# Optimization experiments

Hardware: AMD Instinct MI355X
Metric: run time of the kernel (lower is better)

The kernel has to match this reference:

```python
import jax, jax.numpy as jnp
import numpy as np

GRADIENT_SCALE = 1.0  # undefined global in the source; standard surrogate scale
ALPHA = 0.9
BETA = 0.8
THRESHOLD = 1.0
FEATURES = 512
UNITS = 1024
TIME = 256
BATCH = 128

@jax.custom_vjp
def heaviside(x):
    return jnp.where(x > 0, jnp.ones_like(x), jnp.zeros_like(x))

def _heaviside_fwd(x):
    return heaviside(x), x

def _heaviside_bwd(x, dy):
    # dy * GRADIENT_SCALE * (1/(|x|+1))^2  (surrogate gradient from tf.custom_gradient)
    return (dy * (GRADIENT_SCALE * jnp.square(1.0 / (jnp.abs(x) + 1.0))),)

heaviside.defvjp(_heaviside_fwd, _heaviside_bwd)


def setup_inputs() -> dict:
    key = jax.random.key(0)
    k1, k2 = jax.random.split(key)
    inputs = jax.random.normal(k1, (BATCH, FEATURES, TIME), dtype=jnp.float32)
    # keras add_weight default initializer ~ glorot_uniform; any float init is fine for a numerics baseline
    limit = np.sqrt(6.0 / (FEATURES + UNITS)).astype(np.float32)
    w = jax.random.uniform(k2, (FEATURES, UNITS), dtype=jnp.float32, minval=-limit, maxval=limit)
    return {"inputs": inputs, "w": w}


def reference(inputs, w):
    # In the original tf.while_loop body, membrane_potential, synapse and prev_s are
    # returned UNMODIFIED, so they remain zero for every timestep. The recurrence
    # therefore collapses exactly to, per step t:
    #   h_t = x[:, :, t] @ w
    #   i_t = alpha*0 + h_t = h_t
    #   v_t = (beta*0 + h_t) * (threshold - 0) = h_t * threshold
    #   s_t = heaviside(v_t - threshold)
    # which is timestep-independent and can be computed as one batched GEMM.
    h = jnp.einsum('bft,fu->btu', inputs, w)        # [B, T, U]
    v = (BETA * 0.0 + h) * (THRESHOLD - 0.0)        # state terms are identically zero
    s = heaviside(v - THRESHOLD)                    # [B, T, U]
    return jnp.transpose(s, (0, 2, 1))              # [B, U, T], matching tf transpose perm=[1,2,0]
```

## Files before the change

### kernel.cpp

```cpp
#include <hip/hip_runtime.h>


#define BB 128
#define FF 512
#define TT 256
#define UU 1024

typedef float v4f __attribute__((ext_vector_type(4)));
typedef short v8s __attribute__((ext_vector_type(8)));

__device__ __forceinline__ unsigned short bf16rn(float x) {
    unsigned u = __float_as_uint(x);
    u = u + 0x7FFFu + ((u >> 16) & 1u);
    return (unsigned short)(u >> 16);
}
__device__ __forceinline__ float bf16tof(unsigned short h) {
    return __uint_as_float(((unsigned)h) << 16);
}

__global__ __launch_bounds__(256)
void prepass_kernel(const float* __restrict__ in, const float* __restrict__ w,
                    unsigned short* __restrict__ xth, unsigned short* __restrict__ xtl,
                    unsigned short* __restrict__ wth, unsigned short* __restrict__ wtl) {
    __shared__ float Ls[64][65];

    const int z = blockIdx.z;
    const float* src;
    int srow;
    unsigned short *dh, *dl;
    if (z < BB) {
        src = in + (size_t)z * FF * TT;  srow = TT;
        dh = xth + (size_t)z * TT * FF;  dl = xtl + (size_t)z * TT * FF;
    } else {
        const int s = z - BB;
        src = w + s * 256;               srow = UU;
        dh = wth + (size_t)s * 256 * FF; dl = wtl + (size_t)s * 256 * FF;
    }
    const int f0 = blockIdx.y * 64;
    const int c0 = blockIdx.x * 64;
    const int tid = threadIdx.x;
    const int r  = tid >> 4;
    const int c4 = (tid & 15) * 4;

#pragma unroll
    for (int i = 0; i < 4; i++) {
        const float4 v = *(const float4*)&src[(size_t)(f0 + r + 16 * i) * srow + c0 + c4];
        Ls[r + 16 * i][c4 + 0] = v.x;
        Ls[r + 16 * i][c4 + 1] = v.y;
        Ls[r + 16 * i][c4 + 2] = v.z;
        Ls[r + 16 * i][c4 + 3] = v.w;
    }
    __syncthreads();

#pragma unroll
    for (int i = 0; i < 4; i++) {
        const int orow = r + 16 * i;
        float a0 = Ls[c4 + 0][orow];
        float a1 = Ls[c4 + 1][orow];
        float a2 = Ls[c4 + 2][orow];
        float a3 = Ls[c4 + 3][orow];
        unsigned short h0 = bf16rn(a0), h1 = bf16rn(a1), h2 = bf16rn(a2), h3 = bf16rn(a3);
        float l0f = a0 - bf16tof(h0);
        float l1f = a1 - bf16tof(h1);
        float l2f = a2 - bf16tof(h2);
        float l3f = a3 - bf16tof(h3);
        unsigned short l0 = bf16rn(l0f), l1 = bf16rn(l1f), l2 = bf16rn(l2f), l3 = bf16rn(l3f);
        unsigned long long hp = (unsigned long long)h0 | ((unsigned long long)h1 << 16)
                              | ((unsigned long long)h2 << 32) | ((unsigned long long)h3 << 48);
        unsigned long long lp = (unsigned long long)l0 | ((unsigned long long)l1 << 16)
                              | ((unsigned long long)l2 << 32) | ((unsigned long long)l3 << 48);
        const size_t o = (size_t)(c0 + orow) * FF + f0 + c4;
        *(unsigned long long*)&dh[o] = hp;
        *(unsigned long long*)&dl[o] = lp;
    }
}

#define GLL(g, l) __builtin_amdgcn_global_load_lds(                     \
    (const __attribute__((address_space(1))) void*)(g),                 \
    (__attribute__((address_space(3))) void*)(l), 16, 0, 0)

__global__ __launch_bounds__(256, 3)
void snn_mfma_kernel(const unsigned short* __restrict__ wth,
                     const unsigned short* __restrict__ wtl,
                     const unsigned short* __restrict__ xth,
                     const unsigned short* __restrict__ xtl,
                     const float* __restrict__ in, const float* __restrict__ w,
                     float* __restrict__ out) {
    __shared__ unsigned short smem[4 * 128 * 32];

    const int h = blockIdx.x;
    const int l = ((h & 7) << 8) | (h >> 3);
    const int b  = l >> 4;
    const int u0 = ((l >> 1) & 7) * 128;
    const int t0 = (l & 1) * 128;

    const int tid = threadIdx.x;
    const int wv  = tid >> 6;
    const int ln  = tid & 63;
    const int lr  = ln & 15;
    const int lq  = ln >> 4;
    const int wm  = (wv & 1) * 64;
    const int wn  = (wv >> 1) * 64;

    const char* gbase;
    if      (wv == 0) gbase = (const char*)wth + (size_t)u0 * (FF * 2);
    else if (wv == 1) gbase = (const char*)wtl + (size_t)u0 * (FF * 2);
    else if (wv == 2) gbase = (const char*)xth + ((size_t)b * TT + t0) * (FF * 2);
    else              gbase = (const char*)xtl + ((size_t)b * TT + t0) * (FF * 2);
    const int lrow = ln >> 2;
    const int lseg = (((ln & 3) ^ ((lrow >> 1) & 3)) * 16);

    unsigned short* lbase = &smem[wv * 4096];

    v4f acc[4][4];
#pragma unroll
    for (int i = 0; i < 4; i++)
#pragma unroll
        for (int j = 0; j < 4; j++) {
            v4f zz = {0.0f, 0.0f, 0.0f, 0.0f};
            acc[i][j] = zz;
        }

    const int ksel = (lq ^ ((lr >> 1) & 3)) * 8;

    for (int f0 = 0; f0 < FF; f0 += 32) {
#pragma unroll
        for (int s = 0; s < 8; s++) {
            const char* ga = gbase + (size_t)(s * 16 + lrow) * (FF * 2) + f0 * 2 + lseg;
            GLL(ga, (char*)lbase + s * 1024);
        }
        __syncthreads();

        v8s ah[4], al[4], bh[4], bl[4];
#pragma unroll
        for (int i = 0; i < 4; i++) {
            const int ra = (wm + i * 16 + lr) * 32 + ksel;
            ah[i] = *(const v8s*)&smem[ra];
            al[i] = *(const v8s*)&smem[4096 + ra];
        }
#pragma unroll
        for (int j = 0; j < 4; j++) {
            const int rb = (wn + j * 16 + lr) * 32 + ksel;
            bh[j] = *(const v8s*)&smem[8192 + rb];
            bl[j] = *(const v8s*)&smem[12288 + rb];
        }
#pragma unroll
        for (int i = 0; i < 4; i++)
#pragma unroll
            for (int j = 0; j < 4; j++) {
                acc[i][j] = __builtin_amdgcn_mfma_f32_16x16x32_bf16(ah[i], bh[j], acc[i][j], 0, 0, 0);
                acc[i][j] = __builtin_amdgcn_mfma_f32_16x16x32_bf16(ah[i], bl[j], acc[i][j], 0, 0, 0);
                acc[i][j] = __builtin_amdgcn_mfma_f32_16x16x32_bf16(al[i], bh[j], acc[i][j], 0, 0, 0);
            }
        __syncthreads();
    }

    const float* xb   = in  + (size_t)b * FF * TT;
    float* __restrict__ outb = out + (size_t)b * UU * TT;
#pragma unroll
    for (int i = 0; i < 4; i++) {
#pragma unroll
        for (int r = 0; r < 4; r++) {
            const int u = u0 + wm + i * 16 + lq * 4 + r;
#pragma unroll
            for (int j = 0; j < 4; j++) {
                const int t = t0 + wn + j * 16 + lr;
                float hh = acc[i][j][r];
                if (__builtin_expect(__builtin_fabsf(hh - 1.0f) <= 1e-3f, 0)) {
                    float s2 = 0.0f;
                    const float* wp = w  + u;
                    const float* xp = xb + t;
#pragma unroll 16
                    for (int f = 0; f < FF; f++)
                        s2 = fmaf(wp[(size_t)f * UU], xp[(size_t)f * TT], s2);
                    hh = s2;
                }
                outb[(size_t)u * TT + t] = hh > 1.0f ? 1.0f : 0.0f;
            }
        }
    }
}

__global__ __launch_bounds__(256, 4)
void snn_gemm_kernel(const float* __restrict__ in, const float* __restrict__ w,
                     float* __restrict__ out) {
    __shared__ float As[16][128];
    __shared__ float Bs[16][128];

    const int b  = blockIdx.z;
    const int u0 = blockIdx.y * 128;
    const int t0 = blockIdx.x * 128;

    const float* __restrict__ inb  = in  + (size_t)b * FF * TT;
    float* __restrict__       outb = out + (size_t)b * UU * TT;

    const int tid = threadIdx.x;
    const int tx  = tid & 15;
    const int ty  = tid >> 4;

    const int k0 = tid >> 5;
    const int c0 = (tid & 31) * 4;
    const int k1 = k0 + 8;

    float acc[8][8];
#pragma unroll
    for (int i = 0; i < 8; i++)
#pragma unroll
        for (int j = 0; j < 8; j++) acc[i][j] = 0.0f;

    float4 a_r0 = *(const float4*)&w[(size_t)k0 * UU + u0 + c0];
    float4 a_r1 = *(const float4*)&w[(size_t)k1 * UU + u0 + c0];
    float4 b_r0 = *(const float4*)&inb[k0 * TT + t0 + c0];
    float4 b_r1 = *(const float4*)&inb[k1 * TT + t0 + c0];

    for (int f0 = 0; f0 < FF; f0 += 16) {
        *(float4*)&As[k0][c0] = a_r0;
        *(float4*)&As[k1][c0] = a_r1;
        *(float4*)&Bs[k0][c0] = b_r0;
        *(float4*)&Bs[k1][c0] = b_r1;
        __syncthreads();

        if (f0 + 16 < FF) {
            const int fn = f0 + 16;
            a_r0 = *(const float4*)&w[(size_t)(fn + k0) * UU + u0 + c0];
            a_r1 = *(const float4*)&w[(size_t)(fn + k1) * UU + u0 + c0];
            b_r0 = *(const float4*)&inb[(fn + k0) * TT + t0 + c0];
            b_r1 = *(const float4*)&inb[(fn + k1) * TT + t0 + c0];
        }

#pragma unroll
        for (int k = 0; k < 16; k++) {
            const float4 a0 = *(const float4*)&As[k][ty * 4];
            const float4 a1 = *(const float4*)&As[k][ty * 4 + 64];
            const float4 v0 = *(const float4*)&Bs[k][tx * 4];
            const float4 v1 = *(const float4*)&Bs[k][tx * 4 + 64];
            const float am[8] = {a0.x, a0.y, a0.z, a0.w, a1.x, a1.y, a1.z, a1.w};
            const float bn[8] = {v0.x, v0.y, v0.z, v0.w, v1.x, v1.y, v1.z, v1.w};
#pragma unroll
            for (int i = 0; i < 8; i++)
#pragma unroll
                for (int j = 0; j < 8; j++)
                    acc[i][j] = fmaf(am[i], bn[j], acc[i][j]);
        }
        __syncthreads();
    }

#pragma unroll
    for (int i = 0; i < 8; i++) {
        const int m = (i < 4) ? (ty * 4 + i) : (64 + ty * 4 + i - 4);
        float* __restrict__ orow = outb + (size_t)(u0 + m) * TT + t0;
        float4 o0, o1;
        o0.x = acc[i][0] > 1.0f ? 1.0f : 0.0f;
        o0.y = acc[i][1] > 1.0f ? 1.0f : 0.0f;
        o0.z = acc[i][2] > 1.0f ? 1.0f : 0.0f;
        o0.w = acc[i][3] > 1.0f ? 1.0f : 0.0f;
        o1.x = acc[i][4] > 1.0f ? 1.0f : 0.0f;
        o1.y = acc[i][5] > 1.0f ? 1.0f : 0.0f;
        o1.z = acc[i][6] > 1.0f ? 1.0f : 0.0f;
        o1.w = acc[i][7] > 1.0f ? 1.0f : 0.0f;
        *(float4*)&orow[tx * 4]      = o0;
        *(float4*)&orow[tx * 4 + 64] = o1;
    }
}

extern "C" void kernel_launch(void* const* d_in, const int* in_sizes, int n_in,
                              void* d_out, int out_size, void* d_ws, size_t ws_size,
                              hipStream_t stream) {
    const float* in = (const float*)d_in[0];
    const float* w  = (const float*)d_in[1];
    float* out      = (float*)d_out;

    const size_t XN  = (size_t)BB * TT * FF;
    const size_t WN  = (size_t)UU * FF;
    const size_t NEED = (2 * XN + 2 * WN) * sizeof(unsigned short);

    if (ws_size >= NEED) {
        unsigned short* xth = (unsigned short*)d_ws;
        unsigned short* xtl = xth + XN;
        unsigned short* wth = xtl + XN;
        unsigned short* wtl = wth + WN;
        prepass_kernel<<<dim3(4, 8, 132), dim3(256), 0, stream>>>(in, w, xth, xtl, wth, wtl);
        snn_mfma_kernel<<<dim3(2048), dim3(256), 0, stream>>>(
            wth, wtl, xth, xtl, in, w, out);
    } else {
        snn_gemm_kernel<<<dim3(TT / 128, UU / 128, BB), dim3(256), 0, stream>>>(in, w, out);
    }
}
```

Baseline: 481.6 us.

## Double-buffer LDS staging in MFMA GEMM and vectorize prepass stores

The main kernel gets a second LDS buffer. Asynchronous global-to-LDS loads for the next K chunk are issued while MFMAs run on the current chunk, so memory latency overlaps with compute instead of serializing behind each barrier. Doubling LDS to 64KB per block lowers the occupancy hint from 3 to 2 blocks per CU. The prepass transpose now writes 16-byte vectors of eight bf16 values instead of 8-byte packs.

```diff
diff --git a/kernel.cpp b/kernel.cpp
--- a/kernel.cpp
+++ b/kernel.cpp
@@ -8,6 +8,7 @@
 
 typedef float v4f __attribute__((ext_vector_type(4)));
 typedef short v8s __attribute__((ext_vector_type(8)));
+typedef unsigned short v8us __attribute__((ext_vector_type(8)));
 
 __device__ __forceinline__ unsigned short bf16rn(float x) {
     unsigned u = __float_as_uint(x);
@@ -53,25 +54,20 @@
     __syncthreads();
 
 #pragma unroll
-    for (int i = 0; i < 4; i++) {
-        const int orow = r + 16 * i;
-        float a0 = Ls[c4 + 0][orow];
-        float a1 = Ls[c4 + 1][orow];
-        float a2 = Ls[c4 + 2][orow];
-        float a3 = Ls[c4 + 3][orow];
-        unsigned short h0 = bf16rn(a0), h1 = bf16rn(a1), h2 = bf16rn(a2), h3 = bf16rn(a3);
-        float l0f = a0 - bf16tof(h0);
-        float l1f = a1 - bf16tof(h1);
-        float l2f = a2 - bf16tof(h2);
-        float l3f = a3 - bf16tof(h3);
-        unsigned short l0 = bf16rn(l0f), l1 = bf16rn(l1f), l2 = bf16rn(l2f), l3 = bf16rn(l3f);
-        unsigned long long hp = (unsigned long long)h0 | ((unsigned long long)h1 << 16)
-                              | ((unsigned long long)h2 << 32) | ((unsigned long long)h3 << 48);
-        unsigned long long lp = (unsigned long long)l0 | ((unsigned long long)l1 << 16)
-                              | ((unsigned long long)l2 << 32) | ((unsigned long long)l3 << 48);
-        const size_t o = (size_t)(c0 + orow) * FF + f0 + c4;
-        *(unsigned long long*)&dh[o] = hp;
-        *(unsigned long long*)&dl[o] = lp;
+    for (int i = 0; i < 2; i++) {
+        const int orow = 32 * i + (tid >> 3);
+        const int fs   = (tid & 7) * 8;
+        v8us hp, lp;
+#pragma unroll
+        for (int k = 0; k < 8; k++) {
+            const float a = Ls[fs + k][orow];
+            const unsigned short h = bf16rn(a);
+            hp[k] = h;
+            lp[k] = bf16rn(a - bf16tof(h));
+        }
+        const size_t o = (size_t)(c0 + orow) * FF + f0 + fs;
+        *(v8us*)&dh[o] = hp;
+        *(v8us*)&dl[o] = lp;
     }
 }
 
@@ -79,14 +75,48 @@
     (const __attribute__((address_space(1))) void*)(g),                 \
     (__attribute__((address_space(3))) void*)(l), 16, 0, 0)
 
-__global__ __launch_bounds__(256, 3)
+__device__ __forceinline__ void stage_chunk(const char* gbase, unsigned short* lbase,
+                                            int fbyte, int lrow, int lseg) {
+#pragma unroll
+    for (int s = 0; s < 8; s++) {
+        const char* ga = gbase + (size_t)(s * 16 + lrow) * (FF * 2) + fbyte + lseg;
+        GLL(ga, (char*)lbase + s * 1024);
+    }
+}
+
+__device__ __forceinline__ void compute_chunk(const unsigned short* S, v4f acc[4][4],
+                                              int wm, int wn, int lr, int ksel) {
+    v8s ah[4], al[4], bh[4], bl[4];
+#pragma unroll
+    for (int i = 0; i < 4; i++) {
+        const int ra = (wm + i * 16 + lr) * 32 + ksel;
+        ah[i] = *(const v8s*)&S[ra];
+        al[i] = *(const v8s*)&S[4096 + ra];
+    }
+#pragma unroll
+    for (int j = 0; j < 4; j++) {
+        const int rb = (wn + j * 16 + lr) * 32 + ksel;
+        bh[j] = *(const v8s*)&S[8192 + rb];
+        bl[j] = *(const v8s*)&S[12288 + rb];
+    }
+#pragma unroll
+    for (int i = 0; i < 4; i++)
+#pragma unroll
+        for (int j = 0; j < 4; j++) {
+            acc[i][j] = __builtin_amdgcn_mfma_f32_16x16x32_bf16(ah[i], bh[j], acc[i][j], 0, 0, 0);
+            acc[i][j] = __builtin_amdgcn_mfma_f32_16x16x32_bf16(ah[i], bl[j], acc[i][j], 0, 0, 0);
+            acc[i][j] = __builtin_amdgcn_mfma_f32_16x16x32_bf16(al[i], bh[j], acc[i][j], 0, 0, 0);
+        }
+}
+
+__global__ __launch_bounds__(256, 2)
 void snn_mfma_kernel(const unsigned short* __restrict__ wth,
                      const unsigned short* __restrict__ wtl,
                      const unsigned short* __restrict__ xth,
                      const unsigned short* __restrict__ xtl,
                      const float* __restrict__ in, const float* __restrict__ w,
                      float* __restrict__ out) {
-    __shared__ unsigned short smem[4 * 128 * 32];
+    __shared__ unsigned short smem[2][4 * 128 * 32];
 
     const int h = blockIdx.x;
     const int l = ((h & 7) << 8) | (h >> 3);
@@ -110,7 +140,8 @@
     const int lrow = ln >> 2;
     const int lseg = (((ln & 3) ^ ((lrow >> 1) & 3)) * 16);
 
-    unsigned short* lbase = &smem[wv * 4096];
+    unsigned short* lb0 = &smem[0][wv * 4096];
+    unsigned short* lb1 = &smem[1][wv * 4096];
 
     v4f acc[4][4];
 #pragma unroll
@@ -123,35 +154,16 @@
 
     const int ksel = (lq ^ ((lr >> 1) & 3)) * 8;
 
-    for (int f0 = 0; f0 < FF; f0 += 32) {
-#pragma unroll
-        for (int s = 0; s < 8; s++) {
-            const char* ga = gbase + (size_t)(s * 16 + lrow) * (FF * 2) + f0 * 2 + lseg;
-            GLL(ga, (char*)lbase + s * 1024);
-        }
+    stage_chunk(gbase, lb0, 0, lrow, lseg);
+    __syncthreads();
+
+    for (int t = 0; t < 16; t += 2) {
+        stage_chunk(gbase, lb1, (t + 1) * 64, lrow, lseg);
+        compute_chunk(smem[0], acc, wm, wn, lr, ksel);
         __syncthreads();
-
-        v8s ah[4], al[4], bh[4], bl[4];
-#pragma unroll
-        for (int i = 0; i < 4; i++) {
-            const int ra = (wm + i * 16 + lr) * 32 + ksel;
-            ah[i] = *(const v8s*)&smem[ra];
-            al[i] = *(const v8s*)&smem[4096 + ra];
-        }
-#pragma unroll
-        for (int j = 0; j < 4; j++) {
-            const int rb = (wn + j * 16 + lr) * 32 + ksel;
-            bh[j] = *(const v8s*)&smem[8192 + rb];
-            bl[j] = *(const v8s*)&smem[12288 + rb];
-        }
-#pragma unroll
-        for (int i = 0; i < 4; i++)
-#pragma unroll
-            for (int j = 0; j < 4; j++) {
-                acc[i][j] = __builtin_amdgcn_mfma_f32_16x16x32_bf16(ah[i], bh[j], acc[i][j], 0, 0, 0);
-                acc[i][j] = __builtin_amdgcn_mfma_f32_16x16x32_bf16(ah[i], bl[j], acc[i][j], 0, 0, 0);
-                acc[i][j] = __builtin_amdgcn_mfma_f32_16x16x32_bf16(al[i], bh[j], acc[i][j], 0, 0, 0);
-            }
+        if (t + 2 < 16)
+            stage_chunk(gbase, lb0, (t + 2) * 64, lrow, lseg);
+        compute_chunk(smem[1], acc, wm, wn, lr, ksel);
         __syncthreads();
     }
 
```

Measured after the change: 610.9 us. +26.8%, slower.
